# Kernel tuning notes

Measured on AMD Instinct MI355X. Metric: run time of the kernel, lower is better.

Reference implementation:

```python
import jax, jax.numpy as jnp
import numpy as np

# Model constants (match init_kwargs)
H, P, N, G, NL, K = 32, 64, 128, 1, 15, 4   # heads, head_dim, state, groups, lambda levels, conv width
HID, T, BATCH = 1024, 1024, 1
INTER = H * P                    # 2048
CONV_DIM = INTER + 2 * G * N     # 2304
PROJ = INTER + CONV_DIM + H * (NL + 1)  # 4864
EPS = 1e-5


def _level_matrix(t_len: int) -> np.ndarray:
    """Fenwick-tree level assignment: for query t, prefix [0,t] splits into
    power-of-two segments from binary expansion of t+1; segment of length 2^l -> level l."""
    lm = np.zeros((t_len, t_len), dtype=np.int32)
    for t in range(t_len):
        n = t + 1
        while n > 0:
            lb = n & (-n)
            lm[t, n - lb:n] = lb.bit_length() - 1
            n -= lb
    return lm


def setup_inputs() -> dict:
    key = jax.random.key(0)
    ks = jax.random.split(key, 4)
    return {
        "hidden_states": jax.random.normal(ks[0], (BATCH, T, HID), jnp.float32),
        "in_proj_w": jax.random.normal(ks[1], (PROJ, HID), jnp.float32) / np.sqrt(HID).astype(np.float32),
        "in_proj_b": jnp.zeros((PROJ,), jnp.float32),
        "conv_w": jax.random.normal(ks[2], (CONV_DIM, K), jnp.float32) / np.sqrt(K).astype(np.float32),
        "dt_bias": jnp.ones((H,), jnp.float32),
        "A_log": jnp.log(jnp.arange(1, H + 1, dtype=jnp.float32)),
        "L_param": jnp.ones((H, NL), jnp.float32),
        "D": jnp.ones((H,), jnp.float32),
        "rmsnorm_w": jnp.ones((INTER,), jnp.float32),
        "out_proj_w": jax.random.normal(ks[3], (HID, INTER), jnp.float32) / np.sqrt(INTER).astype(np.float32),
        "out_proj_b": jnp.zeros((HID,), jnp.float32),
        "level_mat": jnp.asarray(_level_matrix(T)),  # (T,T) int32, data-independent
    }


def reference(hidden_states, in_proj_w, in_proj_b, conv_w, dt_bias, A_log,
              L_param, D, rmsnorm_w, out_proj_w, out_proj_b, level_mat):
    b, t, _ = hidden_states.shape
    # in_proj and split: [z | xBC | dt | dl]
    zxbcdtdl = hidden_states @ in_proj_w.T + in_proj_b
    z, xBC, dt, dl = jnp.split(zxbcdtdl, [INTER, INTER + CONV_DIM, INTER + CONV_DIM + H], axis=-1)
    # depthwise causal conv1d (width K) + SiLU
    xp = jnp.pad(xBC, ((0, 0), (K - 1, 0), (0, 0)))
    conv = sum(xp[:, w:w + t, :] * conv_w[:, w] for w in range(K))
    xBC = jax.nn.silu(conv)
    x, Bm, Cm = jnp.split(xBC, [INTER, INTER + G * N], axis=-1)
    x = x.reshape(b, t, H, P)          # v pre-scale
    Bm = Bm.reshape(b, t, G, N)        # keys
    Cm = Cm.reshape(b, t, G, N)        # queries
    dl = dl.reshape(b, t, H, NL)
    # D residual uses unscaled x (matches hmamba_chunk_scan_combined ordering)
    D_res = x * D[None, None, :, None]
    dt = jax.nn.softplus(dt + dt_bias)            # (b,t,H)
    v = x * dt[..., None]                          # (b,t,H,P)
    A = -jnp.exp(A_log)                            # (H,)
    g = A * dt                                     # (b,t,H), per-token log-decay (<=0)
    Ls = jax.nn.softplus(L_param * dl)             # (b,t,H,NL) per-token level scales
    # cumulative log-decay; decay(t,s) = exp(cg_t - cg_s), s<=t
    cg = jnp.cumsum(g, axis=1).transpose(0, 2, 1)  # (b,H,t)
    mask = jnp.tril(jnp.ones((t, t), bool))
    logdecay = jnp.where(mask, cg[:, :, :, None] - cg[:, :, None, :], -jnp.inf)
    decay = jnp.exp(logdecay)                      # (b,H,t,s)
    # hierarchical level scale H[t,s] = Ls[b,t,h, level(t,s)]
    Hmat = jnp.take_along_axis(Ls.transpose(0, 2, 1, 3), level_mat[None, None, :, :], axis=-1)  # (b,H,t,s)
    scores = jnp.einsum('btgn,bsgn->bgts', Cm, Bm)  # (b,G,t,s), G=1 broadcasts over heads
    att = scores * decay * Hmat                     # (b,H,t,s), masked via decay=0
    y = jnp.einsum('bhts,bshp->bthp', att, v) + D_res
    y = y.reshape(b, t, INTER)
    # gated RMSNorm with norm_before_gate=False: normalize(y * silu(z)) * w
    yg = y * jax.nn.silu(z)
    y = yg * jax.lax.rsqrt(jnp.mean(yg * yg, axis=-1, keepdims=True) + EPS) * rmsnorm_w
    return y @ out_proj_w.T + out_proj_b
```

## Files before the change

### kernel.cpp

```cpp
#include <hip/hip_runtime.h>
#include <hip/hip_bf16.h>
#include <math.h>

#define T_LEN 1024
#define HID 1024
#define NHEAD 32
#define HDIM 64
#define NSTATE 128
#define NLVL 15
#define KCONV 4
#define INTER 2048
#define CONV_DIM 2304
#define PROJ 4864
#define EPS 1e-5f
#define TPROJ ((size_t)T_LEN * PROJ)

typedef __attribute__((ext_vector_type(8))) _Float16 half8;
typedef __attribute__((ext_vector_type(4))) float float4v;
typedef unsigned short ushort_t;

__device__ __forceinline__ float softplus_f(float x) {
  return fmaxf(x, 0.f) + log1pf(expf(-fabsf(x)));
}
__device__ __forceinline__ float silu_f(float x) {
  return x / (1.f + expf(-x));
}
__device__ __forceinline__ ushort_t f2h(float f) {
  union { _Float16 h; ushort_t u; } v;
  v.h = (_Float16)f;
  return v.u;
}
__device__ __forceinline__ float h2f(ushort_t u) {
  union { ushort_t u; _Float16 h; } v;
  v.u = u;
  return (float)v.h;
}
__device__ __forceinline__ void gload_lds16(const void* g, void* l) {
  __builtin_amdgcn_global_load_lds(
      (const __attribute__((address_space(1))) void*)g,
      (__attribute__((address_space(3))) void*)l, 16, 0, 0);
}

#define N4_HS  (T_LEN * HID / 4)
#define N4_WI  (PROJ * HID / 4)
#define N4_WO  (HID * INTER / 4)
__global__ __launch_bounds__(256) void prep_f16(
    const float* __restrict__ hs, const float* __restrict__ wi,
    const float* __restrict__ wo, ushort_t* __restrict__ hsb,
    ushort_t* __restrict__ wib, ushort_t* __restrict__ wob) {
  int i = blockIdx.x * 256 + threadIdx.x;
  const float* src; ushort_t* dst; int j;
  if (i < N4_HS)              { src = hs; dst = hsb; j = i; }
  else if (i < N4_HS + N4_WI) { src = wi; dst = wib; j = i - N4_HS; }
  else                        { src = wo; dst = wob; j = i - N4_HS - N4_WI; }
  float4 v = reinterpret_cast<const float4*>(src)[j];
  union { ushort_t u[4]; unsigned long long ll; } o;
  o.u[0] = f2h(v.x); o.u[1] = f2h(v.y); o.u[2] = f2h(v.z); o.u[3] = f2h(v.w);
  reinterpret_cast<unsigned long long*>(dst)[j] = o.ll;
}

__global__ __launch_bounds__(256) void gemm_f16_sk(
    const ushort_t* __restrict__ A, const ushort_t* __restrict__ B,
    ushort_t* __restrict__ Cpart, int M, int N, int K, int Kc) {
  __shared__ ushort_t As[2][128][32];
  __shared__ ushort_t Bs[2][128][32];
  const int tid = threadIdx.x;
  const int w = tid >> 6, L = tid & 63;
  const int n0 = blockIdx.x * 128, m0 = blockIdx.y * 128;
  const int kbeg = blockIdx.z * Kc;
  ushort_t* __restrict__ C = Cpart + (size_t)blockIdx.z * M * N;
  const int mq = (w & 1) * 64, nq = (w >> 1) * 64;
  const int srow = (L >> 2);
  const int sch = (L & 3) * 8;

  float4v acc[4][4];
#pragma unroll
  for (int i = 0; i < 4; ++i)
#pragma unroll
    for (int j = 0; j < 4; ++j) acc[i][j] = (float4v){0.f, 0.f, 0.f, 0.f};

  const int niter = Kc / 32;
  {
    const int kk = kbeg;
#pragma unroll
    for (int j = 0; j < 2; ++j) {
      int r0 = 16 * (w * 2 + j);
      gload_lds16(A + (size_t)(m0 + r0 + srow) * K + kk + sch, &As[0][r0][0]);
      gload_lds16(B + (size_t)(n0 + r0 + srow) * K + kk + sch, &Bs[0][r0][0]);
    }
  }
  for (int it = 0; it < niter; ++it) {
    __syncthreads();
    if (it + 1 < niter) {
      const int kk = kbeg + (it + 1) * 32;
      const int nb = (it + 1) & 1;
#pragma unroll
      for (int j = 0; j < 2; ++j) {
        int r0 = 16 * (w * 2 + j);
        gload_lds16(A + (size_t)(m0 + r0 + srow) * K + kk + sch, &As[nb][r0][0]);
        gload_lds16(B + (size_t)(n0 + r0 + srow) * K + kk + sch, &Bs[nb][r0][0]);
      }
    }
    const int cb = it & 1;
    half8 af[4], bf[4];
#pragma unroll
    for (int t = 0; t < 4; ++t) {
      af[t] = *reinterpret_cast<const half8*>(&As[cb][mq + t * 16 + (L & 15)][(L >> 4) * 8]);
      bf[t] = *reinterpret_cast<const half8*>(&Bs[cb][nq + t * 16 + (L & 15)][(L >> 4) * 8]);
    }
#pragma unroll
    for (int mt = 0; mt < 4; ++mt)
#pragma unroll
      for (int nt = 0; nt < 4; ++nt)
        acc[mt][nt] = __builtin_amdgcn_mfma_f32_16x16x32_f16(af[mt], bf[nt], acc[mt][nt], 0, 0, 0);
  }
  const int qrow = (L >> 4) * 4;
#pragma unroll
  for (int mt = 0; mt < 4; ++mt) {
#pragma unroll
    for (int nt = 0; nt < 4; ++nt) {
      int col = n0 + nq + nt * 16 + (L & 15);
#pragma unroll
      for (int r = 0; r < 4; ++r) {
        int row = m0 + mq + mt * 16 + qrow + r;
        C[(size_t)row * N + col] = f2h(acc[mt][nt][r]);
      }
    }
  }
}

__global__ __launch_bounds__(256) void reduce_out8(const ushort_t* __restrict__ p,
                                                   const float* __restrict__ bias,
                                                   float* __restrict__ out, int MN) {
  int i = blockIdx.x * 256 + threadIdx.x;
  if (i * 8 >= MN) return;
  float o[8] = {0.f, 0.f, 0.f, 0.f, 0.f, 0.f, 0.f, 0.f};
#pragma unroll
  for (int z = 0; z < 8; ++z) {
    half8 v = reinterpret_cast<const half8*>(p + (size_t)z * MN)[i];
#pragma unroll
    for (int j = 0; j < 8; ++j) o[j] += (float)v[j];
  }
  int col = (i * 8) & (HID - 1);
#pragma unroll
  for (int j = 0; j < 8; ++j) o[j] += bias[col + j];
  float4 o0 = {o[0], o[1], o[2], o[3]}, o1 = {o[4], o[5], o[6], o[7]};
  reinterpret_cast<float4*>(out)[i * 2] = o0;
  reinterpret_cast<float4*>(out)[i * 2 + 1] = o1;
}

__global__ __launch_bounds__(64) void scan_g(
    const ushort_t* __restrict__ zh, const float* __restrict__ in_b,
    const float* __restrict__ dt_bias, const float* __restrict__ A_log,
    float* __restrict__ dtb, double* __restrict__ cgd) {
  const int h = blockIdx.x, l = threadIdx.x;
  const int c = INTER + CONV_DIM + h;
  const float bb = in_b[c] + dt_bias[h];
  const float Ae = -expf(A_log[h]);
  double pre[16];
  double acc = 0.0;
#pragma unroll
  for (int i = 0; i < 16; ++i) {
    int t = l * 16 + i;
    size_t o = (size_t)t * PROJ + c;
    float x = h2f(zh[o]) + h2f(zh[TPROJ + o]) + h2f(zh[2 * TPROJ + o]) +
              h2f(zh[3 * TPROJ + o]) + bb;
    float dt = softplus_f(x);
    dtb[t * NHEAD + h] = dt;
    acc += (double)(Ae * dt);
    pre[i] = acc;
  }
  double s = acc;
#pragma unroll
  for (int off = 1; off < 64; off <<= 1) {
    double o = __shfl_up(s, off, 64);
    if (l >= off) s += o;
  }
  const double base = s - acc;
  double* cr = cgd + (size_t)h * T_LEN + l * 16;
#pragma unroll
  for (int i = 0; i < 16; ++i) cr[i] = base + pre[i];
}

__global__ __launch_bounds__(256) void conv_fused(
    const ushort_t* __restrict__ zh, const float* __restrict__ in_b,
    const float* __restrict__ conv_w, const float* __restrict__ dtb,
    const float* __restrict__ Dp, ushort_t* __restrict__ vt,
    float* __restrict__ ybuf, ushort_t* __restrict__ Bb,
    ushort_t* __restrict__ Cb) {
  __shared__ float Xl[67][68];
  __shared__ ushort_t Vl[64][68];
  __shared__ float dtl[64];
  const int tq = blockIdx.x, cy = blockIdx.y;
  const int t0 = tq * 64;
  const int tid = threadIdx.x;
  const int lane = tid & 63, g = tid >> 6;
  const bool vpath = (cy < 32);
  const int c0 = vpath ? cy * 64 : INTER + (cy - 32) * 64;
  if (vpath && tid < 64) dtl[tid] = dtb[(t0 + tid) * NHEAD + cy];

  for (int u = tid; u < 67 * 8; u += 256) {
    int r = u >> 3, c8 = (u & 7) * 8;
    int t = t0 - 3 + r;
    float xs[8];
    if (t >= 0) {
      size_t o = (size_t)t * PROJ + INTER + c0 + c8;
      half8 a = *reinterpret_cast<const half8*>(zh + o);
      half8 b = *reinterpret_cast<const half8*>(zh + TPROJ + o);
      half8 c = *reinterpret_cast<const half8*>(zh + 2 * TPROJ + o);
      half8 d = *reinterpret_cast<const half8*>(zh + 3 * TPROJ + o);
#pragma unroll
      for (int j = 0; j < 8; ++j)
        xs[j] = (float)a[j] + (float)b[j] + (float)c[j] + (float)d[j] +
                in_b[INTER + c0 + c8 + j];
    } else {
#pragma unroll
      for (int j = 0; j < 8; ++j) xs[j] = 0.f;
    }
#pragma unroll
    for (int j = 0; j < 8; ++j) Xl[r][c8 + j] = xs[j];
  }
  __syncthreads();

  const int ccol = c0 + lane;
  const float4 cwv = *reinterpret_cast<const float4*>(conv_w + ccol * KCONV);
  const float Dh = vpath ? Dp[cy] : 0.f;
  float xv[19];
#pragma unroll
  for (int i = 0; i < 19; ++i) xv[i] = Xl[g * 16 + i][lane];
#pragma unroll
  for (int i = 0; i < 16; ++i) {
    float acc = xv[i] * cwv.x + xv[i + 1] * cwv.y + xv[i + 2] * cwv.z + xv[i + 3] * cwv.w;
    float sil = silu_f(acc);
    int tl = g * 16 + i;
    int t = t0 + tl;
    if (vpath) {
      Vl[tl][lane] = f2h(sil * dtl[tl]);
      ybuf[(size_t)t * INTER + c0 + lane] = sil * Dh;
    } else if (ccol < INTER + NSTATE) {
      Bb[t * NSTATE + (ccol - INTER)] = f2h(sil);
    } else {
      Cb[t * NSTATE + (ccol - INTER - NSTATE)] = f2h(sil);
    }
  }
  if (vpath) {
    __syncthreads();
#pragma unroll
    for (int rep = 0; rep < 2; ++rep) {
      int u = tid + 256 * rep;
      int p = u >> 3, t8 = (u & 7) * 8;
      union { ushort_t u16[8]; half8 h; } o;
#pragma unroll
      for (int j = 0; j < 8; ++j) o.u16[j] = Vl[t8 + j][p];
      *reinterpret_cast<half8*>(vt + (size_t)(c0 + p) * T_LEN + t0 + t8) = o.h;
    }
  }
}

__global__ __launch_bounds__(256) void attn_mfma(
    const ushort_t* __restrict__ Bb, const ushort_t* __restrict__ Cb,
    const ushort_t* __restrict__ vt, const double* __restrict__ cgd,
    const ushort_t* __restrict__ zh, const float* __restrict__ in_b,
    const float* __restrict__ L_param, float* __restrict__ ybuf) {
  __shared__ ushort_t Bl[64][136];
  __shared__ ushort_t Vtl[64][72];
  __shared__ ushort_t Sl[64][72];
  __shared__ float Lsl[64][16];
  __shared__ float cgq[64];
  __shared__ float cgs[64];

  const int item = blockIdx.x;
  const int h = item / 40;
  const int rem = item - h * 40;
  int qt, j;
  if (rem < 4)        { qt = rem;                 j = 0; }
  else if (rem < 12)  { qt = 4 + (rem - 4) / 2;   j = (rem - 4) % 2; }
  else if (rem < 24)  { qt = 8 + (rem - 12) / 3;  j = (rem - 12) % 3; }
  else                { qt = 12 + (rem - 24) / 4; j = (rem - 24) % 4; }

  const int tid = threadIdx.x;
  const int w = tid >> 6, L = tid & 63;
  const int tq0 = qt * 64;
  const double* cgh = cgd + (size_t)h * T_LEN;
  const double base = cgh[tq0];

  for (int i = tid; i < 64 * NLVL; i += 256) {
    int r = i / NLVL, l = i - r * NLVL;
    int cc = INTER + CONV_DIM + NHEAD + h * NLVL + l;
    size_t o = (size_t)(tq0 + r) * PROJ + cc;
    float x = h2f(zh[o]) + h2f(zh[TPROJ + o]) + h2f(zh[2 * TPROJ + o]) +
              h2f(zh[3 * TPROJ + o]) + in_b[cc];
    Lsl[r][l] = softplus_f(L_param[h * NLVL + l] * x);
  }
  if (tid < 64) cgq[tid] = (float)(cgh[tq0 + tid] - base);

  half8 cfrag[4];
  {
    const ushort_t* cr = Cb + (size_t)(tq0 + w * 16 + (L & 15)) * NSTATE + (L >> 4) * 8;
#pragma unroll
    for (int ks = 0; ks < 4; ++ks)
      cfrag[ks] = *reinterpret_cast<const half8*>(cr + ks * 32);
  }
  float4v yac[4];
#pragma unroll
  for (int i = 0; i < 4; ++i) yac[i] = (float4v){0.f, 0.f, 0.f, 0.f};

  const int qrow = w * 16 + ((L >> 4) << 2);

  const int st0 = 4 * j;
  const int st1 = min(4 * j + 4, qt + 1);
  for (int st = st0; st < st1; ++st) {
    const int ts0 = st * 64;
    __syncthreads();
#pragma unroll
    for (int i = 0; i < 4; ++i) {
      int u = tid + 256 * i;
      int row = u >> 4, kb = (u & 15) * 8;
      *reinterpret_cast<half8*>(&Bl[row][kb]) =
          *reinterpret_cast<const half8*>(Bb + (size_t)(ts0 + row) * NSTATE + kb);
    }
#pragma unroll
    for (int i = 0; i < 2; ++i) {
      int u = tid + 256 * i;
      int p = u >> 3, sc = (u & 7) * 8;
      *reinterpret_cast<half8*>(&Vtl[p][sc]) =
          *reinterpret_cast<const half8*>(vt + (size_t)(h * HDIM + p) * T_LEN + ts0 + sc);
    }
    if (tid < 64) cgs[tid] = (float)(cgh[ts0 + tid] - base);
    __syncthreads();

    float4v sac[4];
#pragma unroll
    for (int nt = 0; nt < 4; ++nt) sac[nt] = (float4v){0.f, 0.f, 0.f, 0.f};
#pragma unroll
    for (int ks = 0; ks < 4; ++ks) {
#pragma unroll
      for (int nt = 0; nt < 4; ++nt) {
        half8 bfrag = *reinterpret_cast<const half8*>(&Bl[nt * 16 + (L & 15)][ks * 32 + (L >> 4) * 8]);
        sac[nt] = __builtin_amdgcn_mfma_f32_16x16x32_f16(cfrag[ks], bfrag, sac[nt], 0, 0, 0);
      }
    }
#pragma unroll
    for (int nt = 0; nt < 4; ++nt) {
      int s = nt * 16 + (L & 15);
      int sg = ts0 + s;
      float cs = cgs[s];
#pragma unroll
      for (int r = 0; r < 4; ++r) {
        int q = qrow + r;
        int tg = tq0 + q;
        float val = 0.f;
        if (sg <= tg) {
          int lvl = 31 - __clz((unsigned)(sg ^ (tg + 1)));
          val = sac[nt][r] * __expf(cgq[q] - cs) * Lsl[q][lvl];
        }
        Sl[q][s] = f2h(val);
      }
    }
    __builtin_amdgcn_s_waitcnt(0xC07F);
#pragma unroll
    for (int ks = 0; ks < 2; ++ks) {
      half8 af = *reinterpret_cast<const half8*>(&Sl[w * 16 + (L & 15)][ks * 32 + (L >> 4) * 8]);
#pragma unroll
      for (int pt = 0; pt < 4; ++pt) {
        half8 bfv = *reinterpret_cast<const half8*>(&Vtl[pt * 16 + (L & 15)][ks * 32 + (L >> 4) * 8]);
        yac[pt] = __builtin_amdgcn_mfma_f32_16x16x32_f16(af, bfv, yac[pt], 0, 0, 0);
      }
    }
  }
#pragma unroll
  for (int pt = 0; pt < 4; ++pt) {
    int p = pt * 16 + (L & 15);
#pragma unroll
    for (int r = 0; r < 4; ++r) {
      int q = qrow + r;
      atomicAdd(ybuf + (size_t)(tq0 + q) * INTER + h * HDIM + p, yac[pt][r]);
    }
  }
}

__global__ __launch_bounds__(256) void rmsnorm_gate(
    const float* __restrict__ ybuf, const ushort_t* __restrict__ zh,
    const float* __restrict__ in_b, const float* __restrict__ w,
    ushort_t* __restrict__ yhf) {
  __shared__ float red[4];
  const int t = blockIdx.x, tid = threadIdx.x;
  const size_t ro = (size_t)t * PROJ + tid * 8;
  const float* yrow = ybuf + (size_t)t * INTER + tid * 8;
  half8 a = *reinterpret_cast<const half8*>(zh + ro);
  half8 b = *reinterpret_cast<const half8*>(zh + TPROJ + ro);
  half8 c = *reinterpret_cast<const half8*>(zh + 2 * TPROJ + ro);
  half8 d = *reinterpret_cast<const half8*>(zh + 3 * TPROJ + ro);
  float4 y0 = reinterpret_cast<const float4*>(yrow)[0];
  float4 y1 = reinterpret_cast<const float4*>(yrow)[1];
  float yv[8] = {y0.x, y0.y, y0.z, y0.w, y1.x, y1.y, y1.z, y1.w};
  float yg[8];
  float ss = 0.f;
#pragma unroll
  for (int j = 0; j < 8; ++j) {
    float z = (float)a[j] + (float)b[j] + (float)c[j] + (float)d[j] + in_b[tid * 8 + j];
    float g = yv[j] * silu_f(z);
    yg[j] = g;
    ss += g * g;
  }
#pragma unroll
  for (int off = 32; off; off >>= 1) ss += __shfl_down(ss, off, 64);
  if ((tid & 63) == 0) red[tid >> 6] = ss;
  __syncthreads();
  if (tid == 0) red[0] = red[0] + red[1] + red[2] + red[3];
  __syncthreads();
  const float scale = rsqrtf(red[0] / (float)INTER + EPS);
  union { ushort_t u[8]; half8 h; } o;
#pragma unroll
  for (int j = 0; j < 8; ++j) o.u[j] = f2h(yg[j] * scale * w[tid * 8 + j]);
  *reinterpret_cast<half8*>(yhf + (size_t)t * INTER + tid * 8) = o.h;
}

extern "C" void kernel_launch(void* const* d_in, const int* in_sizes, int n_in,
                              void* d_out, int out_size, void* d_ws, size_t ws_size,
                              hipStream_t stream) {
  const float* hs        = (const float*)d_in[0];
  const float* in_proj_w = (const float*)d_in[1];
  const float* in_proj_b = (const float*)d_in[2];
  const float* conv_w    = (const float*)d_in[3];
  const float* dt_bias   = (const float*)d_in[4];
  const float* A_log     = (const float*)d_in[5];
  const float* L_param   = (const float*)d_in[6];
  const float* Dp        = (const float*)d_in[7];
  const float* rms_w     = (const float*)d_in[8];
  const float* out_proj_w= (const float*)d_in[9];
  const float* out_proj_b= (const float*)d_in[10];
  float* out = (float*)d_out;

  char* W = (char*)d_ws;
  size_t off = 0;
  auto alloc = [&](size_t bytes) { void* p = W + off; off = (off + bytes + 255) & ~(size_t)255; return p; };
  double*   cgd = (double*)  alloc((size_t)NHEAD * T_LEN * 8);
  ushort_t* zh  = (ushort_t*)alloc((size_t)4 * TPROJ * 2);
  ushort_t* opp = (ushort_t*)alloc((size_t)8 * T_LEN * HID * 2);
  float*    ybuf= (float*)   alloc((size_t)T_LEN * INTER * 4);
  float*    dtb = (float*)   alloc((size_t)T_LEN * NHEAD * 4);
  ushort_t* hsb = (ushort_t*)alloc((size_t)T_LEN * HID * 2);
  ushort_t* Wib = (ushort_t*)alloc((size_t)PROJ * HID * 2);
  ushort_t* Wob = (ushort_t*)alloc((size_t)HID * INTER * 2);
  ushort_t* yhf = (ushort_t*)alloc((size_t)T_LEN * INTER * 2);
  ushort_t* vt  = (ushort_t*)alloc((size_t)T_LEN * INTER * 2);
  ushort_t* Bb  = (ushort_t*)alloc((size_t)T_LEN * NSTATE * 2);
  ushort_t* Cb  = (ushort_t*)alloc((size_t)T_LEN * NSTATE * 2);

  prep_f16<<<(N4_HS + N4_WI + N4_WO) / 256, 256, 0, stream>>>(
      hs, in_proj_w, out_proj_w, hsb, Wib, Wob);

  gemm_f16_sk<<<dim3(PROJ / 128, T_LEN / 128, 4), 256, 0, stream>>>(
      hsb, Wib, zh, T_LEN, PROJ, HID, HID / 4);

  scan_g<<<NHEAD, 64, 0, stream>>>(zh, in_proj_b, dt_bias, A_log, dtb, cgd);

  conv_fused<<<dim3(T_LEN / 64, 36), 256, 0, stream>>>(
      zh, in_proj_b, conv_w, dtb, Dp, vt, ybuf, Bb, Cb);

  attn_mfma<<<NHEAD * 40, 256, 0, stream>>>(Bb, Cb, vt, cgd, zh, in_proj_b,
                                            L_param, ybuf);

  rmsnorm_gate<<<T_LEN, 256, 0, stream>>>(ybuf, zh, in_proj_b, rms_w, yhf);

  gemm_f16_sk<<<dim3(HID / 128, T_LEN / 128, 8), 256, 0, stream>>>(
      yhf, Wob, opp, T_LEN, HID, INTER, INTER / 8);
  reduce_out8<<<(T_LEN * HID / 8 + 255) / 256, 256, 0, stream>>>(
      opp, out_proj_b, out, T_LEN * HID);
}
```

Before: 201.9 us.

## Keep attention score tile in registers, feed PV MFMA directly without LDS

The QK^T MFMA operands are swapped so each lane's accumulator holds the transposed score fragment. That layout matches the A-operand layout of a 16x16x16 f16 MFMA, so scaled scores go straight from registers into the PV product. This removes the shared-memory score buffer, its write and read-back, and the wait between them. The trade-off is twice as many smaller-K MFMA instructions for PV and a changed per-lane indexing of decay and level scales.

```diff
diff --git a/kernel.cpp b/kernel.cpp
--- a/kernel.cpp
+++ b/kernel.cpp
@@ -16,6 +16,7 @@
 #define TPROJ ((size_t)T_LEN * PROJ)
 
 typedef __attribute__((ext_vector_type(8))) _Float16 half8;
+typedef __attribute__((ext_vector_type(4))) _Float16 half4;
 typedef __attribute__((ext_vector_type(4))) float float4v;
 typedef unsigned short ushort_t;
 
@@ -264,7 +265,6 @@
     const float* __restrict__ L_param, float* __restrict__ ybuf) {
   __shared__ ushort_t Bl[64][136];
   __shared__ ushort_t Vtl[64][72];
-  __shared__ ushort_t Sl[64][72];
   __shared__ float Lsl[64][16];
   __shared__ float cgq[64];
   __shared__ float cgs[64];
@@ -305,7 +305,12 @@
 #pragma unroll
   for (int i = 0; i < 4; ++i) yac[i] = (float4v){0.f, 0.f, 0.f, 0.f};
 
-  const int qrow = w * 16 + ((L >> 4) << 2);
+  __syncthreads();
+  const int qS = w * 16 + (L & 15);
+  const float cq = cgq[qS];
+  const float* Lsq = &Lsl[qS][0];
+  const int tgp1 = tq0 + qS + 1;
+  const int sbase = (L >> 4) * 4;
 
   const int st0 = 4 * j;
   const int st1 = min(4 * j + 4, qt + 1);
@@ -337,37 +342,32 @@
 #pragma unroll
       for (int nt = 0; nt < 4; ++nt) {
         half8 bfrag = *reinterpret_cast<const half8*>(&Bl[nt * 16 + (L & 15)][ks * 32 + (L >> 4) * 8]);
-        sac[nt] = __builtin_amdgcn_mfma_f32_16x16x32_f16(cfrag[ks], bfrag, sac[nt], 0, 0, 0);
+        sac[nt] = __builtin_amdgcn_mfma_f32_16x16x32_f16(bfrag, cfrag[ks], sac[nt], 0, 0, 0);
       }
     }
 #pragma unroll
     for (int nt = 0; nt < 4; ++nt) {
-      int s = nt * 16 + (L & 15);
-      int sg = ts0 + s;
-      float cs = cgs[s];
+      float4 c4 = *reinterpret_cast<const float4*>(&cgs[nt * 16 + sbase]);
+      float cv[4] = {c4.x, c4.y, c4.z, c4.w};
+      half4 sv;
 #pragma unroll
       for (int r = 0; r < 4; ++r) {
-        int q = qrow + r;
-        int tg = tq0 + q;
+        int sg = ts0 + nt * 16 + sbase + r;
         float val = 0.f;
-        if (sg <= tg) {
-          int lvl = 31 - __clz((unsigned)(sg ^ (tg + 1)));
-          val = sac[nt][r] * __expf(cgq[q] - cs) * Lsl[q][lvl];
+        if (sg < tgp1) {
+          int lvl = 31 - __clz((unsigned)(sg ^ tgp1));
+          val = sac[nt][r] * __expf(cq - cv[r]) * Lsq[lvl];
         }
-        Sl[q][s] = f2h(val);
+        sv[r] = (_Float16)val;
       }
-    }
-    __builtin_amdgcn_s_waitcnt(0xC07F);
-#pragma unroll
-    for (int ks = 0; ks < 2; ++ks) {
-      half8 af = *reinterpret_cast<const half8*>(&Sl[w * 16 + (L & 15)][ks * 32 + (L >> 4) * 8]);
 #pragma unroll
       for (int pt = 0; pt < 4; ++pt) {
-        half8 bfv = *reinterpret_cast<const half8*>(&Vtl[pt * 16 + (L & 15)][ks * 32 + (L >> 4) * 8]);
-        yac[pt] = __builtin_amdgcn_mfma_f32_16x16x32_f16(af, bfv, yac[pt], 0, 0, 0);
+        half4 bv = *reinterpret_cast<const half4*>(&Vtl[pt * 16 + (L & 15)][nt * 16 + sbase]);
+        yac[pt] = __builtin_amdgcn_mfma_f32_16x16x16f16(sv, bv, yac[pt], 0, 0, 0);
       }
     }
   }
+  const int qrow = w * 16 + ((L >> 4) << 2);
 #pragma unroll
   for (int pt = 0; pt < 4; ++pt) {
     int p = pt * 16 + (L & 15);
```

New measurement: 202.8 us. About the same (+0.4%).

## Drop LDS staging of B and V tiles in attention, read fragments from global

Applied to the files above, without the earlier changes.

The attention kernel no longer copies B, V^T and the cumulative-decay slices into shared memory each key tile. Each wave now loads its MFMA fragments straight from global memory and computes per-row decay values in registers. The level-scale table is rebuilt so each wave fills only the rows it reads later. This removes both per-tile __syncthreads barriers and the LDS round trip, at the cost of four waves issuing redundant global loads of the same B and V tiles, which rely on L1/L2 hits.

```diff
diff --git a/kernel.cpp b/kernel.cpp
--- a/kernel.cpp
+++ b/kernel.cpp
@@ -16,6 +16,7 @@
 #define TPROJ ((size_t)T_LEN * PROJ)
 
 typedef __attribute__((ext_vector_type(8))) _Float16 half8;
+typedef __attribute__((ext_vector_type(4))) _Float16 half4;
 typedef __attribute__((ext_vector_type(4))) float float4v;
 typedef unsigned short ushort_t;
 
@@ -262,12 +263,8 @@
     const ushort_t* __restrict__ vt, const double* __restrict__ cgd,
     const ushort_t* __restrict__ zh, const float* __restrict__ in_b,
     const float* __restrict__ L_param, float* __restrict__ ybuf) {
-  __shared__ ushort_t Bl[64][136];
-  __shared__ ushort_t Vtl[64][72];
   __shared__ ushort_t Sl[64][72];
   __shared__ float Lsl[64][16];
-  __shared__ float cgq[64];
-  __shared__ float cgs[64];
 
   const int item = blockIdx.x;
   const int h = item / 40;
@@ -284,15 +281,23 @@
   const double* cgh = cgd + (size_t)h * T_LEN;
   const double base = cgh[tq0];
 
-  for (int i = tid; i < 64 * NLVL; i += 256) {
-    int r = i / NLVL, l = i - r * NLVL;
-    int cc = INTER + CONV_DIM + NHEAD + h * NLVL + l;
-    size_t o = (size_t)(tq0 + r) * PROJ + cc;
-    float x = h2f(zh[o]) + h2f(zh[TPROJ + o]) + h2f(zh[2 * TPROJ + o]) +
-              h2f(zh[3 * TPROJ + o]) + in_b[cc];
-    Lsl[r][l] = softplus_f(L_param[h * NLVL + l] * x);
-  }
-  if (tid < 64) cgq[tid] = (float)(cgh[tq0 + tid] - base);
+  {
+    const int row = w * 16 + (L & 15);
+    const int l0 = (L >> 4) * 4;
+    const int cc0 = INTER + CONV_DIM + NHEAD + h * NLVL;
+    const size_t o = (size_t)(tq0 + row) * PROJ + cc0;
+    float vals[4];
+#pragma unroll
+    for (int k = 0; k < 4; ++k) {
+      int l = l0 + k;
+      if (l < NLVL) {
+        float x = h2f(zh[o + l]) + h2f(zh[TPROJ + o + l]) +
+                  h2f(zh[2 * TPROJ + o + l]) + h2f(zh[3 * TPROJ + o + l]) + in_b[cc0 + l];
+        vals[k] = softplus_f(L_param[h * NLVL + l] * x);
+      } else vals[k] = 0.f;
+    }
+    *reinterpret_cast<float4*>(&Lsl[row][l0]) = (float4){vals[0], vals[1], vals[2], vals[3]};
+  }
 
   half8 cfrag[4];
   {
@@ -301,42 +306,30 @@
     for (int ks = 0; ks < 4; ++ks)
       cfrag[ks] = *reinterpret_cast<const half8*>(cr + ks * 32);
   }
+  const int qrow = w * 16 + ((L >> 4) << 2);
+  float cq4[4];
+#pragma unroll
+  for (int r = 0; r < 4; ++r) cq4[r] = (float)(cgh[tq0 + qrow + r] - base);
+
   float4v yac[4];
 #pragma unroll
   for (int i = 0; i < 4; ++i) yac[i] = (float4v){0.f, 0.f, 0.f, 0.f};
 
-  const int qrow = w * 16 + ((L >> 4) << 2);
+  __builtin_amdgcn_s_waitcnt(0xC07F);
 
   const int st0 = 4 * j;
   const int st1 = min(4 * j + 4, qt + 1);
   for (int st = st0; st < st1; ++st) {
     const int ts0 = st * 64;
-    __syncthreads();
-#pragma unroll
-    for (int i = 0; i < 4; ++i) {
-      int u = tid + 256 * i;
-      int row = u >> 4, kb = (u & 15) * 8;
-      *reinterpret_cast<half8*>(&Bl[row][kb]) =
-          *reinterpret_cast<const half8*>(Bb + (size_t)(ts0 + row) * NSTATE + kb);
-    }
-#pragma unroll
-    for (int i = 0; i < 2; ++i) {
-      int u = tid + 256 * i;
-      int p = u >> 3, sc = (u & 7) * 8;
-      *reinterpret_cast<half8*>(&Vtl[p][sc]) =
-          *reinterpret_cast<const half8*>(vt + (size_t)(h * HDIM + p) * T_LEN + ts0 + sc);
-    }
-    if (tid < 64) cgs[tid] = (float)(cgh[ts0 + tid] - base);
-    __syncthreads();
-
     float4v sac[4];
 #pragma unroll
     for (int nt = 0; nt < 4; ++nt) sac[nt] = (float4v){0.f, 0.f, 0.f, 0.f};
 #pragma unroll
-    for (int ks = 0; ks < 4; ++ks) {
-#pragma unroll
-      for (int nt = 0; nt < 4; ++nt) {
-        half8 bfrag = *reinterpret_cast<const half8*>(&Bl[nt * 16 + (L & 15)][ks * 32 + (L >> 4) * 8]);
+    for (int nt = 0; nt < 4; ++nt) {
+      const ushort_t* br = Bb + (size_t)(ts0 + nt * 16 + (L & 15)) * NSTATE + (L >> 4) * 8;
+#pragma unroll
+      for (int ks = 0; ks < 4; ++ks) {
+        half8 bfrag = *reinterpret_cast<const half8*>(br + ks * 32);
         sac[nt] = __builtin_amdgcn_mfma_f32_16x16x32_f16(cfrag[ks], bfrag, sac[nt], 0, 0, 0);
       }
     }
@@ -344,7 +337,7 @@
     for (int nt = 0; nt < 4; ++nt) {
       int s = nt * 16 + (L & 15);
       int sg = ts0 + s;
-      float cs = cgs[s];
+      float cs = (float)(cgh[sg] - base);
 #pragma unroll
       for (int r = 0; r < 4; ++r) {
         int q = qrow + r;
@@ -352,7 +345,7 @@
         float val = 0.f;
         if (sg <= tg) {
           int lvl = 31 - __clz((unsigned)(sg ^ (tg + 1)));
-          val = sac[nt][r] * __expf(cgq[q] - cs) * Lsl[q][lvl];
+          val = sac[nt][r] * __expf(cq4[r] - cs) * Lsl[q][lvl];
         }
         Sl[q][s] = f2h(val);
       }
@@ -363,7 +356,8 @@
       half8 af = *reinterpret_cast<const half8*>(&Sl[w * 16 + (L & 15)][ks * 32 + (L >> 4) * 8]);
 #pragma unroll
       for (int pt = 0; pt < 4; ++pt) {
-        half8 bfv = *reinterpret_cast<const half8*>(&Vtl[pt * 16 + (L & 15)][ks * 32 + (L >> 4) * 8]);
+        half8 bfv = *reinterpret_cast<const half8*>(
+            vt + (size_t)(h * HDIM + pt * 16 + (L & 15)) * T_LEN + ts0 + ks * 32 + (L >> 4) * 8);
         yac[pt] = __builtin_amdgcn_mfma_f32_16x16x32_f16(af, bfv, yac[pt], 0, 0, 0);
       }
     }
```

New measurement: 251.9 us. 1.25x slower.
